# Kernel tuning notes

Measured on AMD Instinct MI355X. Metric: run time of the kernel, lower is better.

## Reference

```python
import jax, jax.numpy as jnp
import numpy as np

B, S, D, E = 8, 2048, 1024, 8


def setup_inputs() -> dict:
    key = jax.random.key(0)
    k1, k2, k3, k4 = jax.random.split(key, 4)
    return {
        "x": jax.random.normal(k1, (B, S, D), dtype=jnp.float32),
        "routing_scores": jax.random.normal(k2, (B, E), dtype=jnp.float32),
        "expert_w": jax.random.normal(k3, (E, D, D), dtype=jnp.float32) / np.sqrt(D),
        "expert_b": jax.random.normal(k4, (E, D), dtype=jnp.float32),
        "k": 2,
    }


def reference(x, routing_scores, expert_w, expert_b, k):
    batch = routing_scores.shape[0]
    # top-k gating mask + renormalization scale (torch.topk + scatter_ equivalent)
    values, indices = jax.lax.top_k(routing_scores, k)              # (B, k)
    mask = jnp.zeros_like(routing_scores, dtype=bool)
    mask = mask.at[jnp.arange(batch)[:, None], indices].set(True)    # (B, E)
    scale = 1.0 / (values.sum(axis=1, keepdims=True) + 1e-8)         # (B, 1)
    masked_scores = scale * routing_scores * mask                    # (B, E)

    # dense per-expert transform: expert_e(x) = x @ W_e + b_e  -> (E, B, S, D)
    expert_out = jnp.einsum("bsd,edf->ebsf", x, expert_w) + expert_b[:, None, None, :]
    # weighted scatter-accumulate over experts (zero weight for inactive pairs)
    final_output = jnp.einsum("be,ebsf->bsf", masked_scores, expert_out)

    return final_output, mask.sum(axis=0)
```

## Files before the change

### kernel.cpp

```cpp
#include <hip/hip_runtime.h>

#define NB 8
#define NS 2048
#define ND 1024
#define NE 8

typedef unsigned short ushort_t;
typedef __attribute__((ext_vector_type(8))) short bf16x8;
typedef __attribute__((ext_vector_type(4))) float f32x4;

__device__ __forceinline__ unsigned short f2bf(float f) {
    union { float f; unsigned int u; } x; x.f = f;
    unsigned int u = x.u + 0x7fffu + ((x.u >> 16) & 1u);
    return (unsigned short)(u >> 16);
}

__device__ __forceinline__ void gload16(const void* g, void* l) {
    __builtin_amdgcn_global_load_lds(
        (const __attribute__((address_space(1))) unsigned int*)g,
        (__attribute__((address_space(3))) unsigned int*)l, 16, 0, 0);
}

__global__ void routing_kernel(const float* __restrict__ scores,
                               const int* __restrict__ kp,
                               float* __restrict__ coef,
                               float* __restrict__ counts) {
    __shared__ int selS[NB][NE];
    int t = threadIdx.x;
    int k = *kp;
    if (t < NB) {
        float s[NE];
#pragma unroll
        for (int e = 0; e < NE; ++e) s[e] = scores[t * NE + e];
        bool sel[NE];
#pragma unroll
        for (int e = 0; e < NE; ++e) sel[e] = false;
        float sum = 0.f;
        for (int j = 0; j < k; ++j) {
            int best = 0; float bv = -3.4e38f;
#pragma unroll
            for (int e = 0; e < NE; ++e)
                if (!sel[e] && s[e] > bv) { bv = s[e]; best = e; }
            sel[best] = true; sum += bv;
        }
        float scale = 1.f / (sum + 1e-8f);
#pragma unroll
        for (int e = 0; e < NE; ++e) {
            coef[t * NE + e] = sel[e] ? scale * s[e] : 0.f;
            selS[t][e] = sel[e] ? 1 : 0;
        }
    }
    __syncthreads();
    if (t < NE) {
        int c = 0;
#pragma unroll
        for (int b = 0; b < NB; ++b) c += selS[b][t];
        counts[t] = (float)c;
    }
}

__global__ void bias_kernel(const float* __restrict__ eb,
                            const float* __restrict__ coef,
                            float* __restrict__ bias) {
    int b = blockIdx.y;
    int f = blockIdx.x * 256 + threadIdx.x;
    float acc = 0.f;
#pragma unroll
    for (int e = 0; e < NE; ++e) {
        float c = coef[b * NE + e];
        if (c != 0.f) acc += c * eb[e * ND + f];
    }
    bias[b * ND + f] = acc;
}

__global__ void combine_kernel(const float* __restrict__ W,
                               const float* __restrict__ coef,
                               ushort_t* __restrict__ wct) {
    __shared__ float tile[64][65];
    int b = blockIdx.z;
    int d0 = blockIdx.y * 64, f0 = blockIdx.x * 64;
    int t = threadIdx.x;
    int lr = t >> 4;
    int lc = (t & 15) * 4;
    float4 acc[4];
#pragma unroll
    for (int it = 0; it < 4; ++it) acc[it] = make_float4(0.f, 0.f, 0.f, 0.f);
#pragma unroll
    for (int e = 0; e < NE; ++e) {
        float c = coef[b * NE + e];
        if (c != 0.f) {
            const float* We = W + ((size_t)e * ND * ND);
#pragma unroll
            for (int it = 0; it < 4; ++it) {
                int d = d0 + lr + it * 16;
                float4 v = *(const float4*)(We + (size_t)d * ND + f0 + lc);
                acc[it].x += c * v.x; acc[it].y += c * v.y;
                acc[it].z += c * v.z; acc[it].w += c * v.w;
            }
        }
    }
#pragma unroll
    for (int it = 0; it < 4; ++it) {
        int r = lr + it * 16;
        tile[r][lc + 0] = acc[it].x; tile[r][lc + 1] = acc[it].y;
        tile[r][lc + 2] = acc[it].z; tile[r][lc + 3] = acc[it].w;
    }
    __syncthreads();
    int dl = t & 63;
    int frow = t >> 6;
    ushort_t* dst = wct + (size_t)b * ND * ND + (size_t)f0 * ND + d0 + dl;
#pragma unroll
    for (int it = 0; it < 16; ++it) {
        int f = frow + it * 4;
        dst[(size_t)f * ND] = f2bf(tile[dl][f]);
    }
}

__global__ void convert_kernel(const float* __restrict__ x, ushort_t* __restrict__ xb) {
    int i = blockIdx.x * 256 + threadIdx.x;
    const float4* p = (const float4*)x + 2 * (size_t)i;
    float4 a = p[0], b = p[1];
    uint4 o;
    o.x = (unsigned)f2bf(a.x) | ((unsigned)f2bf(a.y) << 16);
    o.y = (unsigned)f2bf(a.z) | ((unsigned)f2bf(a.w) << 16);
    o.z = (unsigned)f2bf(b.x) | ((unsigned)f2bf(b.y) << 16);
    o.w = (unsigned)f2bf(b.z) | ((unsigned)f2bf(b.w) << 16);
    ((uint4*)xb)[i] = o;
}

__global__ __launch_bounds__(512, 2) void gemm_kernel(const ushort_t* __restrict__ xb,
                                                      const ushort_t* __restrict__ wct,
                                                      const float* __restrict__ bias,
                                                      float* __restrict__ out) {
    __shared__ ushort_t ldsA[2][256 * 64];
    __shared__ ushort_t ldsB[2][256 * 64];

    int bid = blockIdx.x;
    int b = bid & 7;
    int tile = bid >> 3;
    int m0 = (tile >> 2) * 256;
    int n0 = (tile & 3) * 256;
    const ushort_t* A  = xb  + ((size_t)b * NS * ND) + (size_t)m0 * ND;
    const ushort_t* Bt = wct + ((size_t)b * ND * ND) + (size_t)n0 * ND;

    int t = threadIdx.x, lane = t & 63, wave = t >> 6;
    int wm = wave >> 2, wn = wave & 3;
    int fr = lane & 15, fq = lane >> 4;

    int srow = lane >> 3;
    int sslot = (lane & 7) ^ srow;
    const ushort_t* gA[4];
    const ushort_t* gB[4];
#pragma unroll
    for (int i = 0; i < 4; ++i) {
        int r = (i * 8 + wave) * 8 + srow;
        gA[i] = A  + (size_t)r * ND + sslot * 8;
        gB[i] = Bt + (size_t)r * ND + sslot * 8;
    }

    int slotr = (fq ^ (fr & 7)) * 16;
    int aoff[8], boff[4];
#pragma unroll
    for (int mi = 0; mi < 8; ++mi) aoff[mi] = (wm * 128 + mi * 16 + fr) * 128 + slotr;
#pragma unroll
    for (int nj = 0; nj < 4; ++nj) boff[nj] = (wn * 64 + nj * 16 + fr) * 128 + slotr;

    f32x4 acc[8][4];
#pragma unroll
    for (int i = 0; i < 8; ++i)
#pragma unroll
        for (int j = 0; j < 4; ++j) acc[i][j] = (f32x4){0.f, 0.f, 0.f, 0.f};

    const int NT = ND / 64;

#pragma unroll
    for (int i = 0; i < 4; ++i) {
        gload16(gA[i], (char*)&ldsA[0][0] + (i * 8 + wave) * 1024);
        gA[i] += 64;
    }
#pragma unroll
    for (int i = 0; i < 4; ++i) {
        gload16(gB[i], (char*)&ldsB[0][0] + (i * 8 + wave) * 1024);
        gB[i] += 64;
    }
    asm volatile("s_waitcnt vmcnt(0)" ::: "memory");
    __builtin_amdgcn_s_barrier();

    for (int kt = 0; kt < NT; ++kt) {
        const char* lA = (const char*)&ldsA[kt & 1][0];
        const char* lB = (const char*)&ldsB[kt & 1][0];
        bool pre = (kt + 1 < NT);
        char* dA = (char*)&ldsA[(kt + 1) & 1][0];
        char* dB = (char*)&ldsB[(kt + 1) & 1][0];

        __builtin_amdgcn_sched_barrier(0);
        bf16x8 bf0[4], bf1[4], a0[4], a1[4], a2[4], a3[4];
#pragma unroll
        for (int nj = 0; nj < 4; ++nj) bf0[nj] = *(const bf16x8*)(lB + boff[nj]);
#pragma unroll
        for (int mi = 0; mi < 4; ++mi) a0[mi] = *(const bf16x8*)(lA + aoff[mi]);
#pragma unroll
        for (int nj = 0; nj < 4; ++nj) bf1[nj] = *(const bf16x8*)(lB + (boff[nj] ^ 64));
#pragma unroll
        for (int mi = 0; mi < 4; ++mi) a1[mi] = *(const bf16x8*)(lA + aoff[mi + 4]);
        if (pre) {
#pragma unroll
            for (int i = 0; i < 4; ++i) {
                gload16(gA[i], dA + (i * 8 + wave) * 1024);
                gA[i] += 64;
            }
        }
        __builtin_amdgcn_sched_barrier(0);
        asm volatile("s_waitcnt lgkmcnt(8)" ::: "memory");
        __builtin_amdgcn_sched_barrier(0);
        __builtin_amdgcn_s_setprio(1);
#pragma unroll
        for (int mi = 0; mi < 4; ++mi)
#pragma unroll
            for (int nj = 0; nj < 4; ++nj)
                acc[mi][nj] = __builtin_amdgcn_mfma_f32_16x16x32_bf16(a0[mi], bf0[nj], acc[mi][nj], 0, 0, 0);
        __builtin_amdgcn_s_setprio(0);
#pragma unroll
        for (int mi = 0; mi < 4; ++mi) a2[mi] = *(const bf16x8*)(lA + (aoff[mi] ^ 64));
        if (pre) {
#pragma unroll
            for (int i = 0; i < 4; ++i) {
                gload16(gB[i], dB + (i * 8 + wave) * 1024);
                gB[i] += 64;
            }
        }
        __builtin_amdgcn_sched_barrier(0);
        asm volatile("s_waitcnt lgkmcnt(4)" ::: "memory");
        __builtin_amdgcn_sched_barrier(0);
        __builtin_amdgcn_s_setprio(1);
#pragma unroll
        for (int mi = 0; mi < 4; ++mi)
#pragma unroll
            for (int nj = 0; nj < 4; ++nj)
                acc[mi + 4][nj] = __builtin_amdgcn_mfma_f32_16x16x32_bf16(a1[mi], bf0[nj], acc[mi + 4][nj], 0, 0, 0);
        __builtin_amdgcn_s_setprio(0);
#pragma unroll
        for (int mi = 0; mi < 4; ++mi) a3[mi] = *(const bf16x8*)(lA + (aoff[mi + 4] ^ 64));
        __builtin_amdgcn_sched_barrier(0);
        asm volatile("s_waitcnt lgkmcnt(4)" ::: "memory");
        __builtin_amdgcn_sched_barrier(0);
        __builtin_amdgcn_s_setprio(1);
#pragma unroll
        for (int mi = 0; mi < 4; ++mi)
#pragma unroll
            for (int nj = 0; nj < 4; ++nj)
                acc[mi][nj] = __builtin_amdgcn_mfma_f32_16x16x32_bf16(a2[mi], bf1[nj], acc[mi][nj], 0, 0, 0);
        __builtin_amdgcn_s_setprio(0);
        __builtin_amdgcn_sched_barrier(0);
        asm volatile("s_waitcnt lgkmcnt(0)" ::: "memory");
        __builtin_amdgcn_sched_barrier(0);
        __builtin_amdgcn_s_setprio(1);
#pragma unroll
        for (int mi = 0; mi < 4; ++mi)
#pragma unroll
            for (int nj = 0; nj < 4; ++nj)
                acc[mi + 4][nj] = __builtin_amdgcn_mfma_f32_16x16x32_bf16(a3[mi], bf1[nj], acc[mi + 4][nj], 0, 0, 0);
        __builtin_amdgcn_s_setprio(0);
        __builtin_amdgcn_sched_barrier(0);
        if (pre) {
            asm volatile("s_waitcnt vmcnt(0)" ::: "memory");
            __builtin_amdgcn_s_barrier();
        }
    }

    const float* bs = bias + b * ND;
    float* O = out + ((size_t)b * NS * ND);
#pragma unroll
    for (int mi = 0; mi < 8; ++mi) {
        int row = m0 + wm * 128 + mi * 16 + fq * 4;
#pragma unroll
        for (int nj = 0; nj < 4; ++nj) {
            int col = n0 + wn * 64 + nj * 16 + fr;
            float bv = bs[col];
            f32x4 v = acc[mi][nj];
#pragma unroll
            for (int r = 0; r < 4; ++r)
                O[(size_t)(row + r) * ND + col] = v[r] + bv;
        }
    }
}

extern "C" void kernel_launch(void* const* d_in, const int* in_sizes, int n_in,
                              void* d_out, int out_size, void* d_ws, size_t ws_size,
                              hipStream_t stream) {
    const float* x      = (const float*)d_in[0];
    const float* scores = (const float*)d_in[1];
    const float* Wx     = (const float*)d_in[2];
    const float* eb     = (const float*)d_in[3];
    const int*   kp     = (const int*)d_in[4];
    float* out = (float*)d_out;
    char* ws = (char*)d_ws;

    float*    coef  = (float*)(ws);
    float*    bias  = (float*)(ws + 1024);
    ushort_t* xbuf  = (ushort_t*)(ws + 65536);
    ushort_t* wct   = (ushort_t*)(ws + 65536 + (size_t)NB * NS * ND * 2);
    float*    counts = out + (size_t)NB * NS * ND;

    routing_kernel<<<1, 64, 0, stream>>>(scores, kp, coef, counts);
    bias_kernel<<<dim3(ND / 256, NB), 256, 0, stream>>>(eb, coef, bias);
    combine_kernel<<<dim3(ND / 64, ND / 64, NB), 256, 0, stream>>>(Wx, coef, wct);
    convert_kernel<<<dim3(NB * NS * ND / 8 / 256), 256, 0, stream>>>(x, xbuf);
    gemm_kernel<<<256, 512, 0, stream>>>(xbuf, wct, bias, out);
}
```

Measured before the change: 73.84 us.

## Fuse fp32-to-bf16 conversion of activations into GEMM A-tile loading

Removes the separate convert kernel and its bf16 workspace. The GEMM now loads fp32 activations into registers, packs them to bf16 and writes them into swizzled LDS for the next k-tile, while B keeps using direct global-to-LDS loads. This eliminates a full write and re-read of the converted activation buffer and one launch. In exchange it adds register pressure, VALU conversion work in the main loop, and doubles the global bytes read per A tile.

Result: slower. 82.82 us (+12.2%).

```diff
diff --git a/kernel.cpp b/kernel.cpp
--- a/kernel.cpp
+++ b/kernel.cpp
@@ -1,4 +1,5 @@
 #include <hip/hip_runtime.h>
+#include <hip/hip_bf16.h>
 
 #define NB 8
 #define NS 2048
@@ -13,6 +14,11 @@
     union { float f; unsigned int u; } x; x.f = f;
     unsigned int u = x.u + 0x7fffu + ((x.u >> 16) & 1u);
     return (unsigned short)(u >> 16);
+}
+
+__device__ __forceinline__ unsigned pk2(float a, float b) {
+    __hip_bfloat162 h = __float22bfloat162_rn(make_float2(a, b));
+    union { __hip_bfloat162 h; unsigned u; } c; c.h = h; return c.u;
 }
 
 __device__ __forceinline__ void gload16(const void* g, void* l) {
@@ -116,19 +122,7 @@
     }
 }
 
-__global__ void convert_kernel(const float* __restrict__ x, ushort_t* __restrict__ xb) {
-    int i = blockIdx.x * 256 + threadIdx.x;
-    const float4* p = (const float4*)x + 2 * (size_t)i;
-    float4 a = p[0], b = p[1];
-    uint4 o;
-    o.x = (unsigned)f2bf(a.x) | ((unsigned)f2bf(a.y) << 16);
-    o.y = (unsigned)f2bf(a.z) | ((unsigned)f2bf(a.w) << 16);
-    o.z = (unsigned)f2bf(b.x) | ((unsigned)f2bf(b.y) << 16);
-    o.w = (unsigned)f2bf(b.z) | ((unsigned)f2bf(b.w) << 16);
-    ((uint4*)xb)[i] = o;
-}
-
-__global__ __launch_bounds__(512, 2) void gemm_kernel(const ushort_t* __restrict__ xb,
+__global__ __launch_bounds__(512, 2) void gemm_kernel(const float* __restrict__ x,
                                                       const ushort_t* __restrict__ wct,
                                                       const float* __restrict__ bias,
                                                       float* __restrict__ out) {
@@ -140,21 +134,25 @@
     int tile = bid >> 3;
     int m0 = (tile >> 2) * 256;
     int n0 = (tile & 3) * 256;
-    const ushort_t* A  = xb  + ((size_t)b * NS * ND) + (size_t)m0 * ND;
+    const float*    A  = x   + ((size_t)b * NS * ND) + (size_t)m0 * ND;
     const ushort_t* Bt = wct + ((size_t)b * ND * ND) + (size_t)n0 * ND;
 
     int t = threadIdx.x, lane = t & 63, wave = t >> 6;
     int wm = wave >> 2, wn = wave & 3;
     int fr = lane & 15, fq = lane >> 4;
 
+    int arow = t >> 1, ah = t & 1;
+    const float* xA = A + (size_t)arow * ND;
+    ushort_t* wA[2];
+#pragma unroll
+    for (int bb = 0; bb < 2; ++bb) wA[bb] = &ldsA[bb][0] + arow * 64;
+
     int srow = lane >> 3;
     int sslot = (lane & 7) ^ srow;
-    const ushort_t* gA[4];
     const ushort_t* gB[4];
 #pragma unroll
     for (int i = 0; i < 4; ++i) {
         int r = (i * 8 + wave) * 8 + srow;
-        gA[i] = A  + (size_t)r * ND + sslot * 8;
         gB[i] = Bt + (size_t)r * ND + sslot * 8;
     }
 
@@ -173,25 +171,35 @@
 
     const int NT = ND / 64;
 
-#pragma unroll
-    for (int i = 0; i < 4; ++i) {
-        gload16(gA[i], (char*)&ldsA[0][0] + (i * 8 + wave) * 1024);
-        gA[i] += 64;
-    }
-#pragma unroll
-    for (int i = 0; i < 4; ++i) {
-        gload16(gB[i], (char*)&ldsB[0][0] + (i * 8 + wave) * 1024);
-        gB[i] += 64;
-    }
-    asm volatile("s_waitcnt vmcnt(0)" ::: "memory");
-    __builtin_amdgcn_s_barrier();
+    {
+        float4 pa[8];
+#pragma unroll
+        for (int j = 0; j < 4; ++j) {
+            pa[j * 2]     = *(const float4*)(xA + (ah * 4 + j) * 8);
+            pa[j * 2 + 1] = *(const float4*)(xA + (ah * 4 + j) * 8 + 4);
+        }
+#pragma unroll
+        for (int i = 0; i < 4; ++i)
+            gload16(gB[i], (char*)&ldsB[0][0] + (i * 8 + wave) * 1024);
+#pragma unroll
+        for (int j = 0; j < 4; ++j) {
+            uint4 o;
+            o.x = pk2(pa[j * 2].x, pa[j * 2].y);
+            o.y = pk2(pa[j * 2].z, pa[j * 2].w);
+            o.z = pk2(pa[j * 2 + 1].x, pa[j * 2 + 1].y);
+            o.w = pk2(pa[j * 2 + 1].z, pa[j * 2 + 1].w);
+            *(uint4*)(wA[0] + ((ah * 4 + j) ^ (arow & 7)) * 8) = o;
+        }
+        asm volatile("s_waitcnt vmcnt(0) lgkmcnt(0)" ::: "memory");
+        __builtin_amdgcn_s_barrier();
+    }
 
     for (int kt = 0; kt < NT; ++kt) {
         const char* lA = (const char*)&ldsA[kt & 1][0];
         const char* lB = (const char*)&ldsB[kt & 1][0];
         bool pre = (kt + 1 < NT);
-        char* dA = (char*)&ldsA[(kt + 1) & 1][0];
-        char* dB = (char*)&ldsB[(kt + 1) & 1][0];
+        int nb = (kt + 1) & 1;
+        char* dB = (char*)&ldsB[nb][0];
 
         __builtin_amdgcn_sched_barrier(0);
         bf16x8 bf0[4], bf1[4], a0[4], a1[4], a2[4], a3[4];
@@ -203,11 +211,13 @@
         for (int nj = 0; nj < 4; ++nj) bf1[nj] = *(const bf16x8*)(lB + (boff[nj] ^ 64));
 #pragma unroll
         for (int mi = 0; mi < 4; ++mi) a1[mi] = *(const bf16x8*)(lA + aoff[mi + 4]);
+        float4 pa[8];
         if (pre) {
-#pragma unroll
-            for (int i = 0; i < 4; ++i) {
-                gload16(gA[i], dA + (i * 8 + wave) * 1024);
-                gA[i] += 64;
+            const float* xk = xA + (kt + 1) * 64;
+#pragma unroll
+            for (int j = 0; j < 4; ++j) {
+                pa[j * 2]     = *(const float4*)(xk + (ah * 4 + j) * 8);
+                pa[j * 2 + 1] = *(const float4*)(xk + (ah * 4 + j) * 8 + 4);
             }
         }
         __builtin_amdgcn_sched_barrier(0);
@@ -225,8 +235,8 @@
         if (pre) {
 #pragma unroll
             for (int i = 0; i < 4; ++i) {
+                gB[i] += 64;
                 gload16(gB[i], dB + (i * 8 + wave) * 1024);
-                gB[i] += 64;
             }
         }
         __builtin_amdgcn_sched_barrier(0);
@@ -263,7 +273,19 @@
         __builtin_amdgcn_s_setprio(0);
         __builtin_amdgcn_sched_barrier(0);
         if (pre) {
-            asm volatile("s_waitcnt vmcnt(0)" ::: "memory");
+            asm volatile("s_waitcnt vmcnt(4)" ::: "memory");
+            __builtin_amdgcn_sched_barrier(0);
+#pragma unroll
+            for (int j = 0; j < 4; ++j) {
+                uint4 o;
+                o.x = pk2(pa[j * 2].x, pa[j * 2].y);
+                o.y = pk2(pa[j * 2].z, pa[j * 2].w);
+                o.z = pk2(pa[j * 2 + 1].x, pa[j * 2 + 1].y);
+                o.w = pk2(pa[j * 2 + 1].z, pa[j * 2 + 1].w);
+                *(uint4*)(wA[nb] + ((ah * 4 + j) ^ (arow & 7)) * 8) = o;
+            }
+            __builtin_amdgcn_sched_barrier(0);
+            asm volatile("s_waitcnt vmcnt(0) lgkmcnt(0)" ::: "memory");
             __builtin_amdgcn_s_barrier();
         }
     }
@@ -298,13 +320,11 @@
 
     float*    coef  = (float*)(ws);
     float*    bias  = (float*)(ws + 1024);
-    ushort_t* xbuf  = (ushort_t*)(ws + 65536);
-    ushort_t* wct   = (ushort_t*)(ws + 65536 + (size_t)NB * NS * ND * 2);
+    ushort_t* wct   = (ushort_t*)(ws + 65536);
     float*    counts = out + (size_t)NB * NS * ND;
 
     routing_kernel<<<1, 64, 0, stream>>>(scores, kp, coef, counts);
     bias_kernel<<<dim3(ND / 256, NB), 256, 0, stream>>>(eb, coef, bias);
     combine_kernel<<<dim3(ND / 64, ND / 64, NB), 256, 0, stream>>>(Wx, coef, wct);
-    convert_kernel<<<dim3(NB * NS * ND / 8 / 256), 256, 0, stream>>>(x, xbuf);
-    gemm_kernel<<<256, 512, 0, stream>>>(xbuf, wct, bias, out);
-}
+    gemm_kernel<<<256, 512, 0, stream>>>(x, wct, bias, out);
+}
```

## Shrink GEMM tile to 256x128 and use triple-buffered LDS prefetch

Applied to the files above, without the earlier changes.

Changes the GEMM block tile from 256x256 to 256x128, which doubles the grid to 512 blocks, and gives each wave a 64x64 sub-tile instead of 128x64. LDS goes from double to triple buffering, so global-to-LDS loads are issued two k-steps ahead and the vmcnt waits allow outstanding loads. The aim is better fill across the 256 CUs (the old 256-block grid gives one block per CU) and more latency hiding. In exchange, each block reuses less data, so more global traffic is needed per FLOP, and each wave does fewer MFMAs per LDS read.

Measured after the change: 75.40 us. +2.1%, slower.

```diff
diff --git a/kernel.cpp b/kernel.cpp
--- a/kernel.cpp
+++ b/kernel.cpp
@@ -132,83 +132,83 @@
                                                       const ushort_t* __restrict__ wct,
                                                       const float* __restrict__ bias,
                                                       float* __restrict__ out) {
-    __shared__ ushort_t ldsA[2][256 * 64];
-    __shared__ ushort_t ldsB[2][256 * 64];
+    __shared__ ushort_t ldsA[3][256 * 64];
+    __shared__ ushort_t ldsB[3][128 * 64];
 
     int bid = blockIdx.x;
     int b = bid & 7;
     int tile = bid >> 3;
-    int m0 = (tile >> 2) * 256;
-    int n0 = (tile & 3) * 256;
+    int m0 = (tile >> 3) * 256;
+    int n0 = (tile & 7) * 128;
     const ushort_t* A  = xb  + ((size_t)b * NS * ND) + (size_t)m0 * ND;
     const ushort_t* Bt = wct + ((size_t)b * ND * ND) + (size_t)n0 * ND;
 
     int t = threadIdx.x, lane = t & 63, wave = t >> 6;
-    int wm = wave >> 2, wn = wave & 3;
+    int wm = wave >> 1, wn = wave & 1;
     int fr = lane & 15, fq = lane >> 4;
 
     int srow = lane >> 3;
     int sslot = (lane & 7) ^ srow;
     const ushort_t* gA[4];
-    const ushort_t* gB[4];
-#pragma unroll
-    for (int i = 0; i < 4; ++i) {
-        int r = (i * 8 + wave) * 8 + srow;
-        gA[i] = A  + (size_t)r * ND + sslot * 8;
-        gB[i] = Bt + (size_t)r * ND + sslot * 8;
-    }
+    const ushort_t* gB[2];
+#pragma unroll
+    for (int i = 0; i < 4; ++i)
+        gA[i] = A  + (size_t)(wave * 32 + i * 8 + srow) * ND + sslot * 8;
+#pragma unroll
+    for (int i = 0; i < 2; ++i)
+        gB[i] = Bt + (size_t)(wave * 16 + i * 8 + srow) * ND + sslot * 8;
 
     int slotr = (fq ^ (fr & 7)) * 16;
-    int aoff[8], boff[4];
-#pragma unroll
-    for (int mi = 0; mi < 8; ++mi) aoff[mi] = (wm * 128 + mi * 16 + fr) * 128 + slotr;
+    int aoff[4], boff[4];
+#pragma unroll
+    for (int mi = 0; mi < 4; ++mi) aoff[mi] = (wm * 64 + mi * 16 + fr) * 128 + slotr;
 #pragma unroll
     for (int nj = 0; nj < 4; ++nj) boff[nj] = (wn * 64 + nj * 16 + fr) * 128 + slotr;
 
-    f32x4 acc[8][4];
-#pragma unroll
-    for (int i = 0; i < 8; ++i)
+    f32x4 acc[4][4];
+#pragma unroll
+    for (int i = 0; i < 4; ++i)
 #pragma unroll
         for (int j = 0; j < 4; ++j) acc[i][j] = (f32x4){0.f, 0.f, 0.f, 0.f};
 
     const int NT = ND / 64;
 
 #pragma unroll
-    for (int i = 0; i < 4; ++i) {
-        gload16(gA[i], (char*)&ldsA[0][0] + (i * 8 + wave) * 1024);
-        gA[i] += 64;
-    }
-#pragma unroll
-    for (int i = 0; i < 4; ++i) {
-        gload16(gB[i], (char*)&ldsB[0][0] + (i * 8 + wave) * 1024);
-        gB[i] += 64;
-    }
-    asm volatile("s_waitcnt vmcnt(0)" ::: "memory");
+    for (int T = 0; T < 2; ++T) {
+#pragma unroll
+        for (int i = 0; i < 4; ++i)
+            gload16(gA[i] + T * 64, &ldsA[T][(wave * 32 + i * 8) * 64]);
+#pragma unroll
+        for (int i = 0; i < 2; ++i)
+            gload16(gB[i] + T * 64, &ldsB[T][(wave * 16 + i * 8) * 64]);
+    }
+    asm volatile("s_waitcnt vmcnt(6)" ::: "memory");
     __builtin_amdgcn_s_barrier();
 
+    int cur = 0;
     for (int kt = 0; kt < NT; ++kt) {
-        const char* lA = (const char*)&ldsA[kt & 1][0];
-        const char* lB = (const char*)&ldsB[kt & 1][0];
-        bool pre = (kt + 1 < NT);
-        char* dA = (char*)&ldsA[(kt + 1) & 1][0];
-        char* dB = (char*)&ldsB[(kt + 1) & 1][0];
-
-        __builtin_amdgcn_sched_barrier(0);
-        bf16x8 bf0[4], bf1[4], a0[4], a1[4], a2[4], a3[4];
-#pragma unroll
-        for (int nj = 0; nj < 4; ++nj) bf0[nj] = *(const bf16x8*)(lB + boff[nj]);
+        const char* lA = (const char*)&ldsA[cur][0];
+        const char* lB = (const char*)&ldsB[cur][0];
+        int sq = cur + 2; if (sq >= 3) sq -= 3;
+
+        __builtin_amdgcn_sched_barrier(0);
+        bf16x8 b0[4], a0[4], b1[4], a1[4];
+#pragma unroll
+        for (int nj = 0; nj < 4; ++nj) b0[nj] = *(const bf16x8*)(lB + boff[nj]);
 #pragma unroll
         for (int mi = 0; mi < 4; ++mi) a0[mi] = *(const bf16x8*)(lA + aoff[mi]);
 #pragma unroll
-        for (int nj = 0; nj < 4; ++nj) bf1[nj] = *(const bf16x8*)(lB + (boff[nj] ^ 64));
-#pragma unroll
-        for (int mi = 0; mi < 4; ++mi) a1[mi] = *(const bf16x8*)(lA + aoff[mi + 4]);
-        if (pre) {
-#pragma unroll
-            for (int i = 0; i < 4; ++i) {
-                gload16(gA[i], dA + (i * 8 + wave) * 1024);
-                gA[i] += 64;
-            }
+        for (int nj = 0; nj < 4; ++nj) b1[nj] = *(const bf16x8*)(lB + (boff[nj] ^ 64));
+#pragma unroll
+        for (int mi = 0; mi < 4; ++mi) a1[mi] = *(const bf16x8*)(lA + (aoff[mi] ^ 64));
+        if (kt + 2 < NT) {
+            int ko = (kt + 2) * 64;
+#pragma unroll
+            for (int i = 0; i < 4; ++i)
+                gload16(gA[i] + ko, &ldsA[sq][(wave * 32 + i * 8) * 64]);
+#pragma unroll
+            for (int i = 0; i < 2; ++i)
+                gload16(gB[i] + ko, &ldsB[sq][(wave * 16 + i * 8) * 64]);
         }
         __builtin_amdgcn_sched_barrier(0);
         asm volatile("s_waitcnt lgkmcnt(8)" ::: "memory");
@@ -218,61 +218,33 @@
         for (int mi = 0; mi < 4; ++mi)
 #pragma unroll
             for (int nj = 0; nj < 4; ++nj)
-                acc[mi][nj] = __builtin_amdgcn_mfma_f32_16x16x32_bf16(a0[mi], bf0[nj], acc[mi][nj], 0, 0, 0);
+                acc[mi][nj] = __builtin_amdgcn_mfma_f32_16x16x32_bf16(a0[mi], b0[nj], acc[mi][nj], 0, 0, 0);
         __builtin_amdgcn_s_setprio(0);
-#pragma unroll
-        for (int mi = 0; mi < 4; ++mi) a2[mi] = *(const bf16x8*)(lA + (aoff[mi] ^ 64));
-        if (pre) {
-#pragma unroll
-            for (int i = 0; i < 4; ++i) {
-                gload16(gB[i], dB + (i * 8 + wave) * 1024);
-                gB[i] += 64;
-            }
-        }
-        __builtin_amdgcn_sched_barrier(0);
-        asm volatile("s_waitcnt lgkmcnt(4)" ::: "memory");
+        __builtin_amdgcn_sched_barrier(0);
+        asm volatile("s_waitcnt lgkmcnt(0)" ::: "memory");
         __builtin_amdgcn_sched_barrier(0);
         __builtin_amdgcn_s_setprio(1);
 #pragma unroll
         for (int mi = 0; mi < 4; ++mi)
 #pragma unroll
             for (int nj = 0; nj < 4; ++nj)
-                acc[mi + 4][nj] = __builtin_amdgcn_mfma_f32_16x16x32_bf16(a1[mi], bf0[nj], acc[mi + 4][nj], 0, 0, 0);
+                acc[mi][nj] = __builtin_amdgcn_mfma_f32_16x16x32_bf16(a1[mi], b1[nj], acc[mi][nj], 0, 0, 0);
         __builtin_amdgcn_s_setprio(0);
-#pragma unroll
-        for (int mi = 0; mi < 4; ++mi) a3[mi] = *(const bf16x8*)(lA + (aoff[mi + 4] ^ 64));
-        __builtin_amdgcn_sched_barrier(0);
-        asm volatile("s_waitcnt lgkmcnt(4)" ::: "memory");
-        __builtin_amdgcn_sched_barrier(0);
-        __builtin_amdgcn_s_setprio(1);
-#pragma unroll
-        for (int mi = 0; mi < 4; ++mi)
-#pragma unroll
-            for (int nj = 0; nj < 4; ++nj)
-                acc[mi][nj] = __builtin_amdgcn_mfma_f32_16x16x32_bf16(a2[mi], bf1[nj], acc[mi][nj], 0, 0, 0);
-        __builtin_amdgcn_s_setprio(0);
-        __builtin_amdgcn_sched_barrier(0);
-        asm volatile("s_waitcnt lgkmcnt(0)" ::: "memory");
-        __builtin_amdgcn_sched_barrier(0);
-        __builtin_amdgcn_s_setprio(1);
-#pragma unroll
-        for (int mi = 0; mi < 4; ++mi)
-#pragma unroll
-            for (int nj = 0; nj < 4; ++nj)
-                acc[mi + 4][nj] = __builtin_amdgcn_mfma_f32_16x16x32_bf16(a3[mi], bf1[nj], acc[mi + 4][nj], 0, 0, 0);
-        __builtin_amdgcn_s_setprio(0);
-        __builtin_amdgcn_sched_barrier(0);
-        if (pre) {
+        __builtin_amdgcn_sched_barrier(0);
+        if (kt + 2 < NT) {
+            asm volatile("s_waitcnt vmcnt(6)" ::: "memory");
+        } else if (kt + 2 == NT) {
             asm volatile("s_waitcnt vmcnt(0)" ::: "memory");
-            __builtin_amdgcn_s_barrier();
-        }
+        }
+        if (kt + 1 < NT) __builtin_amdgcn_s_barrier();
+        cur += 1; if (cur == 3) cur = 0;
     }
 
     const float* bs = bias + b * ND;
     float* O = out + ((size_t)b * NS * ND);
 #pragma unroll
-    for (int mi = 0; mi < 8; ++mi) {
-        int row = m0 + wm * 128 + mi * 16 + fq * 4;
+    for (int mi = 0; mi < 4; ++mi) {
+        int row = m0 + wm * 64 + mi * 16 + fq * 4;
 #pragma unroll
         for (int nj = 0; nj < 4; ++nj) {
             int col = n0 + wn * 64 + nj * 16 + fr;
@@ -306,5 +278,5 @@
     bias_kernel<<<dim3(ND / 256, NB), 256, 0, stream>>>(eb, coef, bias);
     combine_kernel<<<dim3(ND / 64, ND / 64, NB), 256, 0, stream>>>(Wx, coef, wct);
     convert_kernel<<<dim3(NB * NS * ND / 8 / 256), 256, 0, stream>>>(x, xbuf);
-    gemm_kernel<<<256, 512, 0, stream>>>(xbuf, wct, bias, out);
-}
+    gemm_kernel<<<512, 512, 0, stream>>>(xbuf, wct, bias, out);
+}
```
